# Optimization experiments

Measured on AMD Instinct MI355X. Metric: run time of the kernel, lower is better.

## Reference

```python
import jax, jax.numpy as jnp
import numpy as np

N = 131072   # nodes (flattened batch)
SI, VI = 128, 64   # in_dims
SO, VO = 128, 64   # out_dims
HD = 128           # h_dim


def setup_inputs() -> dict:
    key = jax.random.key(0)
    ks = jax.random.split(key, 8)
    scale = lambda fan_in: 1.0 / np.sqrt(fan_in)
    return {
        "s": jax.random.normal(ks[0], (N, SI), dtype=jnp.float32),
        "V": jax.random.normal(ks[1], (N, VI, 3), dtype=jnp.float32),
        # Linear(vi, h_dim, bias=False): weight [h_dim, vi]
        "W_h": jax.random.uniform(ks[2], (HD, VI), jnp.float32, -scale(VI), scale(VI)),
        # Linear(h_dim, vo, bias=False): weight [vo, h_dim]
        "W_V": jax.random.uniform(ks[3], (VO, HD), jnp.float32, -scale(HD), scale(HD)),
        # Linear(si + h_dim, so)
        "W_s_w": jax.random.uniform(ks[4], (SO, SI + HD), jnp.float32, -scale(SI + HD), scale(SI + HD)),
        "W_s_b": jax.random.uniform(ks[5], (SO,), jnp.float32, -scale(SI + HD), scale(SI + HD)),
        # Linear(so, vo) gate
        "W_g_w": jax.random.uniform(ks[6], (VO, SO), jnp.float32, -scale(SO), scale(SO)),
        "W_g_b": jax.random.uniform(ks[7], (VO,), jnp.float32, -scale(SO), scale(SO)),
    }


def reference(s, V, W_h, W_V, W_s_w, W_s_b, W_g_w, W_g_b):
    # Vh: contract vector-channel dim vi, keep 3 spatial dims -> [N, h_dim, 3]
    Vh = jnp.einsum("nvc,hv->nhc", V, W_h)
    # L2 norm over the 3 spatial dims -> [N, h_dim]
    Vh_norm = jnp.sqrt(jnp.sum(Vh * Vh, axis=-1))
    # V_out: [N, vo, 3]
    V_out = jnp.einsum("nhc,oh->noc", Vh, W_V)
    # scalar path: concat + linear + relu -> [N, so]
    s_cat = jnp.concatenate([s, Vh_norm], axis=-1)
    s_out = jax.nn.relu(s_cat @ W_s_w.T + W_s_b)
    # vector gate: sigmoid(Linear(s_out)) broadcast over spatial dim
    gate = jax.nn.sigmoid(s_out @ W_g_w.T + W_g_b)[..., None]  # [N, vo, 1]
    V_out = V_out * gate
    return s_out, V_out
```

## Files before the change

### kernel.cpp

```cpp
#include <hip/hip_runtime.h>
#include <hip/hip_bf16.h>
#include <math.h>

#define NNODES 131072
#define BN 32

typedef __attribute__((ext_vector_type(8))) short bf16x8;
typedef __attribute__((ext_vector_type(4))) float f32x4;

__device__ short g_w[49152];
__device__ short g_wc[4096];

__device__ __forceinline__ short f2b(float f) {
  union { float f; unsigned u; } x; x.f = f;
  unsigned r = x.u + 0x7fffu + ((x.u >> 16) & 1u);
  return (short)(r >> 16);
}
__device__ __forceinline__ short c2b(float f) {
  __hip_bfloat16 h = __float2bfloat16(f);
  return *reinterpret_cast<short*>(&h);
}

__global__ void prep_kernel(const float* __restrict__ W_h, const float* __restrict__ W_V,
                            const float* __restrict__ W_s_w, const float* __restrict__ W_g_w) {
  int b = blockIdx.x;
  if (b < 48) {
    int i4 = (b * 256 + threadIdx.x) * 4;
    const float* src;
    if (i4 < 8192)       src = W_h   + i4;
    else if (i4 < 40960) src = W_s_w + (i4 - 8192);
    else                 src = W_g_w + (i4 - 40960);
    float4 q = *(const float4*)src;
    short4 p;
    p.x = f2b(q.x); p.y = f2b(q.y); p.z = f2b(q.z); p.w = f2b(q.w);
    *(short4*)(g_w + i4) = p;
  } else {
    int gid = (b - 48) * 256 + threadIdx.x;
    int o  = gid >> 4;
    int v0 = (gid & 15) * 4;
    float a0 = 0.f, a1 = 0.f, a2 = 0.f, a3 = 0.f;
    #pragma unroll 8
    for (int h = 0; h < 128; ++h) {
      float wv = W_V[o * 128 + h];
      float4 wh = *(const float4*)(W_h + h * 64 + v0);
      a0 += wv * wh.x; a1 += wv * wh.y; a2 += wv * wh.z; a3 += wv * wh.w;
    }
    short4 p;
    p.x = f2b(a0); p.y = f2b(a1); p.z = f2b(a2); p.w = f2b(a3);
    *(short4*)(g_wc + o * 64 + v0) = p;
  }
}


__global__ __launch_bounds__(256, 3)
void gvp_kernel(const float* __restrict__ s_in, const float* __restrict__ V_in,
                const float* __restrict__ W_s_b, const float* __restrict__ W_g_b,
                float* __restrict__ s_out_g, float* __restrict__ V_out_g)
{
  __shared__ __align__(16) char smem[36864];
  char*  const Vt   = smem;
  float* const VST  = (float*)smem;
  char*  const SCN  = smem + 12288;
  char*  const SOUT = smem + 28672;

  const short* const g_wh = g_w;
  const short* const g_ws = g_w + 8192;
  const short* const g_wg = g_w + 40960;

  const int t    = threadIdx.x;
  const int lane = t & 63;
  const int w    = t >> 6;
  const int l15  = lane & 15;
  const int lk8  = (lane >> 4) << 3;
  const int r4   = (lane >> 4) << 2;
  const long n0  = (long)blockIdx.x * BN;

  {
    const int nl = t >> 3;
    const int vg = t & 7;
    const int v0 = vg << 3;
    const float* vp = V_in + (n0 + nl) * 192 + v0 * 3;
    float fl[24];
    #pragma unroll
    for (int i = 0; i < 6; ++i) *(float4*)(fl + 4 * i) = *(const float4*)(vp + 4 * i);
    #pragma unroll
    for (int c = 0; c < 3; ++c) {
      int row = (c << 5) + nl;
      bf16x8 p;
      #pragma unroll
      for (int j = 0; j < 8; ++j) p[j] = c2b(fl[j * 3 + c]);
      unsigned a = (unsigned)(row * 128) + (((unsigned)(v0 * 2)) ^ (unsigned)((row & 7) << 4));
      *(bf16x8*)(Vt + a) = p;
    }
  }
  {
    const int nl = t >> 3;
    const int kg = t & 7;
    const int k0 = kg << 4;
    const float* sp = s_in + (n0 + nl) * 128 + k0;
    float4 q0 = *(const float4*)(sp);
    float4 q1 = *(const float4*)(sp + 4);
    float4 q2 = *(const float4*)(sp + 8);
    float4 q3 = *(const float4*)(sp + 12);
    bf16x8 pa, pb;
    pa[0] = c2b(q0.x); pa[1] = c2b(q0.y); pa[2] = c2b(q0.z); pa[3] = c2b(q0.w);
    pa[4] = c2b(q1.x); pa[5] = c2b(q1.y); pa[6] = c2b(q1.z); pa[7] = c2b(q1.w);
    pb[0] = c2b(q2.x); pb[1] = c2b(q2.y); pb[2] = c2b(q2.z); pb[3] = c2b(q2.w);
    pb[4] = c2b(q3.x); pb[5] = c2b(q3.y); pb[6] = c2b(q3.z); pb[7] = c2b(q3.w);
    unsigned sw = (unsigned)((nl & 7) << 4);
    *(bf16x8*)(SCN + nl * 512 + (((unsigned)(k0 * 2)) ^ sw))      = pa;
    *(bf16x8*)(SCN + nl * 512 + (((unsigned)(k0 * 2 + 16)) ^ sw)) = pb;
  }
  __syncthreads();

  bf16x8 bf1[2][2];
  #pragma unroll
  for (int cc = 0; cc < 2; ++cc) {
    int h = ((2 * w + cc) << 4) + l15;
    #pragma unroll
    for (int ks = 0; ks < 2; ++ks)
      bf1[cc][ks] = *(const bf16x8*)(g_wh + h * 64 + (ks << 5) + lk8);
  }
  bf16x8 b3[8][2];
  #pragma unroll
  for (int ks = 0; ks < 8; ++ks)
    #pragma unroll
    for (int cc = 0; cc < 2; ++cc) {
      int o = (w << 5) + (cc << 4) + l15;
      b3[ks][cc] = *(const bf16x8*)(g_ws + o * 256 + (ks << 5) + lk8);
    }
  bf16x8 bc[2];
  {
    int o = (w << 4) + l15;
    bc[0] = *(const bf16x8*)(g_wc + o * 64 + lk8);
    bc[1] = *(const bf16x8*)(g_wc + o * 64 + 32 + lk8);
  }

  f32x4 acc1[6][2];
  #pragma unroll
  for (int rt = 0; rt < 6; ++rt) {
    f32x4 z = {0.f, 0.f, 0.f, 0.f};
    acc1[rt][0] = z; acc1[rt][1] = z;
  }
  #pragma unroll
  for (int rt = 0; rt < 6; ++rt) {
    int row = (rt << 4) + l15;
    unsigned sw = (unsigned)((row & 7) << 4);
    bf16x8 af0 = *(const bf16x8*)(Vt + row * 128 + (((unsigned)(lk8 * 2)) ^ sw));
    bf16x8 af1 = *(const bf16x8*)(Vt + row * 128 + (((unsigned)((32 + lk8) * 2)) ^ sw));
    #pragma unroll
    for (int cc = 0; cc < 2; ++cc) {
      acc1[rt][cc] = __builtin_amdgcn_mfma_f32_16x16x32_bf16(af0, bf1[cc][0], acc1[rt][cc], 0, 0, 0);
      acc1[rt][cc] = __builtin_amdgcn_mfma_f32_16x16x32_bf16(af1, bf1[cc][1], acc1[rt][cc], 0, 0, 0);
    }
  }

  #pragma unroll
  for (int cc = 0; cc < 2; ++cc) {
    int col = ((2 * w + cc) << 4) + l15;
    #pragma unroll
    for (int rt = 0; rt < 2; ++rt) {
      #pragma unroll
      for (int i = 0; i < 4; ++i) {
        int nl = (rt << 4) + r4 + i;
        float x0 = acc1[rt][cc][i];
        float x1 = acc1[rt + 2][cc][i];
        float x2 = acc1[rt + 4][cc][i];
        float nrm = sqrtf(x0 * x0 + x1 * x1 + x2 * x2);
        int k = 128 + col;
        unsigned a = (unsigned)(nl * 512) + (((unsigned)(k * 2)) ^ (unsigned)((nl & 7) << 4));
        *(short*)(SCN + a) = c2b(nrm);
      }
    }
  }
  __syncthreads();

  bf16x8 b4[4];
  {
    int o = (w << 4) + l15;
    #pragma unroll
    for (int ks = 0; ks < 4; ++ks)
      b4[ks] = *(const bf16x8*)(g_wg + o * 128 + (ks << 5) + lk8);
  }

  f32x4 acc3[2][2];
  {
    f32x4 z = {0.f, 0.f, 0.f, 0.f};
    acc3[0][0] = z; acc3[0][1] = z; acc3[1][0] = z; acc3[1][1] = z;
  }
  #pragma unroll
  for (int ks = 0; ks < 8; ++ks) {
    #pragma unroll
    for (int rt = 0; rt < 2; ++rt) {
      int row = (rt << 4) + l15;
      unsigned sw = (unsigned)((row & 7) << 4);
      bf16x8 a = *(const bf16x8*)(SCN + row * 512 +
                   (((unsigned)(((ks << 5) + lk8) * 2)) ^ sw));
      acc3[rt][0] = __builtin_amdgcn_mfma_f32_16x16x32_bf16(a, b3[ks][0], acc3[rt][0], 0, 0, 0);
      acc3[rt][1] = __builtin_amdgcn_mfma_f32_16x16x32_bf16(a, b3[ks][1], acc3[rt][1], 0, 0, 0);
    }
  }

  f32x4 acc2[6];
  #pragma unroll
  for (int rt = 0; rt < 6; ++rt) { f32x4 z = {0.f,0.f,0.f,0.f}; acc2[rt] = z; }
  #pragma unroll
  for (int rt = 0; rt < 6; ++rt) {
    int row = (rt << 4) + l15;
    unsigned sw = (unsigned)((row & 7) << 4);
    bf16x8 af0 = *(const bf16x8*)(Vt + row * 128 + (((unsigned)(lk8 * 2)) ^ sw));
    bf16x8 af1 = *(const bf16x8*)(Vt + row * 128 + (((unsigned)((32 + lk8) * 2)) ^ sw));
    acc2[rt] = __builtin_amdgcn_mfma_f32_16x16x32_bf16(af0, bc[0], acc2[rt], 0, 0, 0);
    acc2[rt] = __builtin_amdgcn_mfma_f32_16x16x32_bf16(af1, bc[1], acc2[rt], 0, 0, 0);
  }

  float so[2][2][4];
  {
    float bias0 = W_s_b[(w << 5) + l15];
    float bias1 = W_s_b[(w << 5) + 16 + l15];
    #pragma unroll
    for (int rt = 0; rt < 2; ++rt) {
      #pragma unroll
      for (int i = 0; i < 4; ++i) {
        int row = (rt << 4) + r4 + i;
        unsigned sw = (unsigned)((row & 7) << 4);
        float v0 = fmaxf(acc3[rt][0][i] + bias0, 0.0f);
        float v1 = fmaxf(acc3[rt][1][i] + bias1, 0.0f);
        so[rt][0][i] = v0; so[rt][1][i] = v1;
        int col0 = (w << 5) + l15;
        unsigned a0 = (unsigned)(row * 256) + (((unsigned)(col0 * 2)) ^ sw);
        unsigned a1 = (unsigned)(row * 256) + (((unsigned)((col0 + 16) * 2)) ^ sw);
        *(short*)(SOUT + a0) = c2b(v0);
        *(short*)(SOUT + a1) = c2b(v1);
      }
    }
  }
  __syncthreads();

  f32x4 acc4[2];
  { f32x4 z = {0.f, 0.f, 0.f, 0.f}; acc4[0] = z; acc4[1] = z; }
  #pragma unroll
  for (int ks = 0; ks < 4; ++ks) {
    #pragma unroll
    for (int rt = 0; rt < 2; ++rt) {
      int row = (rt << 4) + l15;
      bf16x8 a = *(const bf16x8*)(SOUT + row * 256 +
                   (((unsigned)(((ks << 5) + lk8) * 2)) ^ ((unsigned)((row & 7) << 4))));
      acc4[rt] = __builtin_amdgcn_mfma_f32_16x16x32_bf16(a, b4[ks], acc4[rt], 0, 0, 0);
    }
  }
  float sg[2][4];
  {
    float biasg = W_g_b[(w << 4) + l15];
    #pragma unroll
    for (int nlg = 0; nlg < 2; ++nlg)
      #pragma unroll
      for (int i = 0; i < 4; ++i)
        sg[nlg][i] = 1.0f / (1.0f + __expf(-(acc4[nlg][i] + biasg)));
  }

  {
    int col = (w << 4) + l15;
    #pragma unroll
    for (int rt = 0; rt < 6; ++rt) {
      int c   = rt >> 1;
      int nlg = rt & 1;
      #pragma unroll
      for (int i = 0; i < 4; ++i) {
        int nl = (nlg << 4) + r4 + i;
        VST[nl * 192 + col * 3 + c] = acc2[rt][i] * sg[nlg][i];
      }
    }
  }
  __syncthreads();

  {
    float4* Vo = (float4*)(V_out_g + n0 * 192);
    const float4* Vs = (const float4*)VST;
    #pragma unroll
    for (int i = 0; i < 6; ++i) {
      int idx = t + 256 * i;
      Vo[idx] = Vs[idx];
    }
  }
  {
    int col0 = (w << 5) + l15;
    #pragma unroll
    for (int rt = 0; rt < 2; ++rt) {
      #pragma unroll
      for (int i = 0; i < 4; ++i) {
        int row = (rt << 4) + r4 + i;
        s_out_g[(n0 + row) * 128 + col0]      = so[rt][0][i];
        s_out_g[(n0 + row) * 128 + col0 + 16] = so[rt][1][i];
      }
    }
  }
}

extern "C" void kernel_launch(void* const* d_in, const int* in_sizes, int n_in,
                              void* d_out, int out_size, void* d_ws, size_t ws_size,
                              hipStream_t stream) {
  const float* s_in  = (const float*)d_in[0];
  const float* V_in  = (const float*)d_in[1];
  const float* W_h   = (const float*)d_in[2];
  const float* W_V   = (const float*)d_in[3];
  const float* W_s_w = (const float*)d_in[4];
  const float* W_s_b = (const float*)d_in[5];
  const float* W_g_w = (const float*)d_in[6];
  const float* W_g_b = (const float*)d_in[7];
  float* out = (float*)d_out;
  float* s_out_g = out;
  float* V_out_g = out + (size_t)NNODES * 128;
  hipLaunchKernelGGL(prep_kernel, dim3(52), dim3(256), 0, stream,
                     W_h, W_V, W_s_w, W_g_w);
  hipLaunchKernelGGL(gvp_kernel, dim3(NNODES / BN), dim3(256), 0, stream,
                     s_in, V_in, W_s_b, W_g_b, s_out_g, V_out_g);
}
```

Baseline: 102.9 us.

## Double node tile to 64 with 8 waves and reshape per-wave work split

Raises the per-block node tile from 32 to 64 and the block size from 256 to 512 threads (8 waves). Each wave now owns one 16-column slice of the hidden and output dims, and the V/gate work is split across wave halves. The concat buffer and the relu-output buffer now share LDS, which needs extra barriers. The V staging buffer gains an XOR swizzle to cut LDS bank conflicts. The goal is to load weight fragments into registers once per 64 nodes instead of 32 and halve the block count, at the cost of more LDS per block (57 KB), two blocks per CU, and more synchronisation.

```diff
diff --git a/kernel.cpp b/kernel.cpp
--- a/kernel.cpp
+++ b/kernel.cpp
@@ -3,7 +3,7 @@
 #include <math.h>
 
 #define NNODES 131072
-#define BN 32
+#define BN 64
 
 typedef __attribute__((ext_vector_type(8))) short bf16x8;
 typedef __attribute__((ext_vector_type(4))) float f32x4;
@@ -52,16 +52,16 @@
 }
 
 
-__global__ __launch_bounds__(256, 3)
+__global__ __launch_bounds__(512, 2)
 void gvp_kernel(const float* __restrict__ s_in, const float* __restrict__ V_in,
                 const float* __restrict__ W_s_b, const float* __restrict__ W_g_b,
                 float* __restrict__ s_out_g, float* __restrict__ V_out_g)
 {
-  __shared__ __align__(16) char smem[36864];
+  __shared__ __align__(16) char smem[57344];
   char*  const Vt   = smem;
   float* const VST  = (float*)smem;
-  char*  const SCN  = smem + 12288;
-  char*  const SOUT = smem + 28672;
+  char*  const SCN  = smem + 24576;
+  char*  const SOUT = smem + 24576;
 
   const short* const g_wh = g_w;
   const short* const g_ws = g_w + 8192;
@@ -70,6 +70,8 @@
   const int t    = threadIdx.x;
   const int lane = t & 63;
   const int w    = t >> 6;
+  const int w4   = w & 3;
+  const int h2   = w >> 2;
   const int l15  = lane & 15;
   const int lk8  = (lane >> 4) << 3;
   const int r4   = (lane >> 4) << 2;
@@ -85,7 +87,7 @@
     for (int i = 0; i < 6; ++i) *(float4*)(fl + 4 * i) = *(const float4*)(vp + 4 * i);
     #pragma unroll
     for (int c = 0; c < 3; ++c) {
-      int row = (c << 5) + nl;
+      int row = (c << 6) + nl;
       bf16x8 p;
       #pragma unroll
       for (int j = 0; j < 8; ++j) p[j] = c2b(fl[j * 3 + c]);
@@ -113,62 +115,51 @@
   }
   __syncthreads();
 
-  bf16x8 bf1[2][2];
-  #pragma unroll
-  for (int cc = 0; cc < 2; ++cc) {
-    int h = ((2 * w + cc) << 4) + l15;
-    #pragma unroll
-    for (int ks = 0; ks < 2; ++ks)
-      bf1[cc][ks] = *(const bf16x8*)(g_wh + h * 64 + (ks << 5) + lk8);
-  }
-  bf16x8 b3[8][2];
-  #pragma unroll
-  for (int ks = 0; ks < 8; ++ks)
-    #pragma unroll
-    for (int cc = 0; cc < 2; ++cc) {
-      int o = (w << 5) + (cc << 4) + l15;
-      b3[ks][cc] = *(const bf16x8*)(g_ws + o * 256 + (ks << 5) + lk8);
-    }
+  bf16x8 bf1[2];
+  {
+    int h = (w << 4) + l15;
+    bf1[0] = *(const bf16x8*)(g_wh + h * 64 + lk8);
+    bf1[1] = *(const bf16x8*)(g_wh + h * 64 + 32 + lk8);
+  }
+  bf16x8 b3[8];
+  {
+    int o = (w << 4) + l15;
+    #pragma unroll
+    for (int ks = 0; ks < 8; ++ks)
+      b3[ks] = *(const bf16x8*)(g_ws + o * 256 + (ks << 5) + lk8);
+  }
   bf16x8 bc[2];
   {
-    int o = (w << 4) + l15;
+    int o = (w4 << 4) + l15;
     bc[0] = *(const bf16x8*)(g_wc + o * 64 + lk8);
     bc[1] = *(const bf16x8*)(g_wc + o * 64 + 32 + lk8);
   }
 
-  f32x4 acc1[6][2];
-  #pragma unroll
-  for (int rt = 0; rt < 6; ++rt) {
-    f32x4 z = {0.f, 0.f, 0.f, 0.f};
-    acc1[rt][0] = z; acc1[rt][1] = z;
-  }
-  #pragma unroll
-  for (int rt = 0; rt < 6; ++rt) {
-    int row = (rt << 4) + l15;
+  f32x4 acc1[12];
+  #pragma unroll
+  for (int r = 0; r < 12; ++r) { f32x4 z = {0.f,0.f,0.f,0.f}; acc1[r] = z; }
+  #pragma unroll
+  for (int r = 0; r < 12; ++r) {
+    int row = (r << 4) + l15;
     unsigned sw = (unsigned)((row & 7) << 4);
     bf16x8 af0 = *(const bf16x8*)(Vt + row * 128 + (((unsigned)(lk8 * 2)) ^ sw));
     bf16x8 af1 = *(const bf16x8*)(Vt + row * 128 + (((unsigned)((32 + lk8) * 2)) ^ sw));
-    #pragma unroll
-    for (int cc = 0; cc < 2; ++cc) {
-      acc1[rt][cc] = __builtin_amdgcn_mfma_f32_16x16x32_bf16(af0, bf1[cc][0], acc1[rt][cc], 0, 0, 0);
-      acc1[rt][cc] = __builtin_amdgcn_mfma_f32_16x16x32_bf16(af1, bf1[cc][1], acc1[rt][cc], 0, 0, 0);
-    }
-  }
-
-  #pragma unroll
-  for (int cc = 0; cc < 2; ++cc) {
-    int col = ((2 * w + cc) << 4) + l15;
-    #pragma unroll
-    for (int rt = 0; rt < 2; ++rt) {
+    acc1[r] = __builtin_amdgcn_mfma_f32_16x16x32_bf16(af0, bf1[0], acc1[r], 0, 0, 0);
+    acc1[r] = __builtin_amdgcn_mfma_f32_16x16x32_bf16(af1, bf1[1], acc1[r], 0, 0, 0);
+  }
+
+  {
+    int col = 128 + (w << 4) + l15;
+    #pragma unroll
+    for (int q = 0; q < 4; ++q) {
       #pragma unroll
       for (int i = 0; i < 4; ++i) {
-        int nl = (rt << 4) + r4 + i;
-        float x0 = acc1[rt][cc][i];
-        float x1 = acc1[rt + 2][cc][i];
-        float x2 = acc1[rt + 4][cc][i];
+        int nl = (q << 4) + r4 + i;
+        float x0 = acc1[q][i];
+        float x1 = acc1[4 + q][i];
+        float x2 = acc1[8 + q][i];
         float nrm = sqrtf(x0 * x0 + x1 * x1 + x2 * x2);
-        int k = 128 + col;
-        unsigned a = (unsigned)(nl * 512) + (((unsigned)(k * 2)) ^ (unsigned)((nl & 7) << 4));
+        unsigned a = (unsigned)(nl * 512) + (((unsigned)(col * 2)) ^ (unsigned)((nl & 7) << 4));
         *(short*)(SCN + a) = c2b(nrm);
       }
     }
@@ -177,121 +168,132 @@
 
   bf16x8 b4[4];
   {
-    int o = (w << 4) + l15;
+    int o = (w4 << 4) + l15;
     #pragma unroll
     for (int ks = 0; ks < 4; ++ks)
       b4[ks] = *(const bf16x8*)(g_wg + o * 128 + (ks << 5) + lk8);
   }
 
-  f32x4 acc3[2][2];
-  {
-    f32x4 z = {0.f, 0.f, 0.f, 0.f};
-    acc3[0][0] = z; acc3[0][1] = z; acc3[1][0] = z; acc3[1][1] = z;
-  }
+  f32x4 acc3[4];
+  #pragma unroll
+  for (int rt = 0; rt < 4; ++rt) { f32x4 z = {0.f,0.f,0.f,0.f}; acc3[rt] = z; }
   #pragma unroll
   for (int ks = 0; ks < 8; ++ks) {
     #pragma unroll
-    for (int rt = 0; rt < 2; ++rt) {
+    for (int rt = 0; rt < 4; ++rt) {
       int row = (rt << 4) + l15;
       unsigned sw = (unsigned)((row & 7) << 4);
       bf16x8 a = *(const bf16x8*)(SCN + row * 512 +
                    (((unsigned)(((ks << 5) + lk8) * 2)) ^ sw));
-      acc3[rt][0] = __builtin_amdgcn_mfma_f32_16x16x32_bf16(a, b3[ks][0], acc3[rt][0], 0, 0, 0);
-      acc3[rt][1] = __builtin_amdgcn_mfma_f32_16x16x32_bf16(a, b3[ks][1], acc3[rt][1], 0, 0, 0);
-    }
-  }
-
-  f32x4 acc2[6];
-  #pragma unroll
-  for (int rt = 0; rt < 6; ++rt) { f32x4 z = {0.f,0.f,0.f,0.f}; acc2[rt] = z; }
-  #pragma unroll
-  for (int rt = 0; rt < 6; ++rt) {
-    int row = (rt << 4) + l15;
-    unsigned sw = (unsigned)((row & 7) << 4);
-    bf16x8 af0 = *(const bf16x8*)(Vt + row * 128 + (((unsigned)(lk8 * 2)) ^ sw));
-    bf16x8 af1 = *(const bf16x8*)(Vt + row * 128 + (((unsigned)((32 + lk8) * 2)) ^ sw));
-    acc2[rt] = __builtin_amdgcn_mfma_f32_16x16x32_bf16(af0, bc[0], acc2[rt], 0, 0, 0);
-    acc2[rt] = __builtin_amdgcn_mfma_f32_16x16x32_bf16(af1, bc[1], acc2[rt], 0, 0, 0);
-  }
-
-  float so[2][2][4];
-  {
-    float bias0 = W_s_b[(w << 5) + l15];
-    float bias1 = W_s_b[(w << 5) + 16 + l15];
-    #pragma unroll
-    for (int rt = 0; rt < 2; ++rt) {
+      acc3[rt] = __builtin_amdgcn_mfma_f32_16x16x32_bf16(a, b3[ks], acc3[rt], 0, 0, 0);
+    }
+  }
+
+  f32x4 acc2[3][2];
+  #pragma unroll
+  for (int c = 0; c < 3; ++c)
+    #pragma unroll
+    for (int j = 0; j < 2; ++j) { f32x4 z = {0.f,0.f,0.f,0.f}; acc2[c][j] = z; }
+  #pragma unroll
+  for (int c = 0; c < 3; ++c) {
+    #pragma unroll
+    for (int j = 0; j < 2; ++j) {
+      int r = c * 4 + 2 * h2 + j;
+      int row = (r << 4) + l15;
+      unsigned sw = (unsigned)((row & 7) << 4);
+      bf16x8 af0 = *(const bf16x8*)(Vt + row * 128 + (((unsigned)(lk8 * 2)) ^ sw));
+      bf16x8 af1 = *(const bf16x8*)(Vt + row * 128 + (((unsigned)((32 + lk8) * 2)) ^ sw));
+      acc2[c][j] = __builtin_amdgcn_mfma_f32_16x16x32_bf16(af0, bc[0], acc2[c][j], 0, 0, 0);
+      acc2[c][j] = __builtin_amdgcn_mfma_f32_16x16x32_bf16(af1, bc[1], acc2[c][j], 0, 0, 0);
+    }
+  }
+
+  float so[4][4];
+  {
+    float bias = W_s_b[(w << 4) + l15];
+    #pragma unroll
+    for (int rt = 0; rt < 4; ++rt)
+      #pragma unroll
+      for (int i = 0; i < 4; ++i)
+        so[rt][i] = fmaxf(acc3[rt][i] + bias, 0.0f);
+  }
+  __syncthreads();
+
+  {
+    int col = (w << 4) + l15;
+    #pragma unroll
+    for (int rt = 0; rt < 4; ++rt) {
       #pragma unroll
       for (int i = 0; i < 4; ++i) {
         int row = (rt << 4) + r4 + i;
-        unsigned sw = (unsigned)((row & 7) << 4);
-        float v0 = fmaxf(acc3[rt][0][i] + bias0, 0.0f);
-        float v1 = fmaxf(acc3[rt][1][i] + bias1, 0.0f);
-        so[rt][0][i] = v0; so[rt][1][i] = v1;
-        int col0 = (w << 5) + l15;
-        unsigned a0 = (unsigned)(row * 256) + (((unsigned)(col0 * 2)) ^ sw);
-        unsigned a1 = (unsigned)(row * 256) + (((unsigned)((col0 + 16) * 2)) ^ sw);
-        *(short*)(SOUT + a0) = c2b(v0);
-        *(short*)(SOUT + a1) = c2b(v1);
+        unsigned a = (unsigned)(row * 256) + (((unsigned)(col * 2)) ^ (unsigned)((row & 7) << 4));
+        *(short*)(SOUT + a) = c2b(so[rt][i]);
       }
     }
   }
   __syncthreads();
 
   f32x4 acc4[2];
-  { f32x4 z = {0.f, 0.f, 0.f, 0.f}; acc4[0] = z; acc4[1] = z; }
+  { f32x4 z = {0.f,0.f,0.f,0.f}; acc4[0] = z; acc4[1] = z; }
   #pragma unroll
   for (int ks = 0; ks < 4; ++ks) {
     #pragma unroll
-    for (int rt = 0; rt < 2; ++rt) {
-      int row = (rt << 4) + l15;
+    for (int j = 0; j < 2; ++j) {
+      int row = ((2 * h2 + j) << 4) + l15;
       bf16x8 a = *(const bf16x8*)(SOUT + row * 256 +
                    (((unsigned)(((ks << 5) + lk8) * 2)) ^ ((unsigned)((row & 7) << 4))));
-      acc4[rt] = __builtin_amdgcn_mfma_f32_16x16x32_bf16(a, b4[ks], acc4[rt], 0, 0, 0);
+      acc4[j] = __builtin_amdgcn_mfma_f32_16x16x32_bf16(a, b4[ks], acc4[j], 0, 0, 0);
     }
   }
   float sg[2][4];
   {
-    float biasg = W_g_b[(w << 4) + l15];
-    #pragma unroll
-    for (int nlg = 0; nlg < 2; ++nlg)
+    float biasg = W_g_b[(w4 << 4) + l15];
+    #pragma unroll
+    for (int j = 0; j < 2; ++j)
       #pragma unroll
       for (int i = 0; i < 4; ++i)
-        sg[nlg][i] = 1.0f / (1.0f + __expf(-(acc4[nlg][i] + biasg)));
-  }
-
+        sg[j][i] = 1.0f / (1.0f + __expf(-(acc4[j][i] + biasg)));
+  }
+  __syncthreads();
+
+  {
+    int col = (w4 << 4) + l15;
+    #pragma unroll
+    for (int c = 0; c < 3; ++c) {
+      #pragma unroll
+      for (int j = 0; j < 2; ++j) {
+        #pragma unroll
+        for (int i = 0; i < 4; ++i) {
+          int nl = ((2 * h2 + j) << 4) + r4 + i;
+          unsigned a = (unsigned)(nl * 768) +
+                       (((unsigned)((col * 3 + c) * 4)) ^ (unsigned)((nl & 7) << 4));
+          *(float*)((char*)VST + a) = acc2[c][j][i] * sg[j][i];
+        }
+      }
+    }
+  }
+  __syncthreads();
+
+  {
+    float4* Vo = (float4*)(V_out_g + n0 * 192);
+    #pragma unroll
+    for (int m = 0; m < 6; ++m) {
+      int f = m * 512 + t;
+      int nl = f / 48;
+      int rem = f - nl * 48;
+      float4 q = *(const float4*)((char*)VST + nl * 768 +
+                   (((unsigned)(rem * 16)) ^ ((unsigned)((nl & 7) << 4))));
+      Vo[f] = q;
+    }
+  }
   {
     int col = (w << 4) + l15;
     #pragma unroll
-    for (int rt = 0; rt < 6; ++rt) {
-      int c   = rt >> 1;
-      int nlg = rt & 1;
+    for (int rt = 0; rt < 4; ++rt) {
       #pragma unroll
       for (int i = 0; i < 4; ++i) {
-        int nl = (nlg << 4) + r4 + i;
-        VST[nl * 192 + col * 3 + c] = acc2[rt][i] * sg[nlg][i];
-      }
-    }
-  }
-  __syncthreads();
-
-  {
-    float4* Vo = (float4*)(V_out_g + n0 * 192);
-    const float4* Vs = (const float4*)VST;
-    #pragma unroll
-    for (int i = 0; i < 6; ++i) {
-      int idx = t + 256 * i;
-      Vo[idx] = Vs[idx];
-    }
-  }
-  {
-    int col0 = (w << 5) + l15;
-    #pragma unroll
-    for (int rt = 0; rt < 2; ++rt) {
-      #pragma unroll
-      for (int i = 0; i < 4; ++i) {
-        int row = (rt << 4) + r4 + i;
-        s_out_g[(n0 + row) * 128 + col0]      = so[rt][0][i];
-        s_out_g[(n0 + row) * 128 + col0 + 16] = so[rt][1][i];
+        int nl = (rt << 4) + r4 + i;
+        s_out_g[(n0 + nl) * 128 + col] = so[rt][i];
       }
     }
   }
@@ -313,6 +315,6 @@
   float* V_out_g = out + (size_t)NNODES * 128;
   hipLaunchKernelGGL(prep_kernel, dim3(52), dim3(256), 0, stream,
                      W_h, W_V, W_s_w, W_g_w);
-  hipLaunchKernelGGL(gvp_kernel, dim3(NNODES / BN), dim3(256), 0, stream,
+  hipLaunchKernelGGL(gvp_kernel, dim3(NNODES / BN), dim3(512), 0, stream,
                      s_in, V_in, W_s_b, W_g_b, s_out_g, V_out_g);
 }
```

Measured after the change: 94.88 us (median of 2 runs). -7.8%, faster.
